# Optimization experiments

Hardware: AMD Instinct MI355X
Metric: run time of the kernel (lower is better)

The kernel has to match this reference:

```python
import jax, jax.numpy as jnp
import numpy as np

B = 4096
FEAT = 512
EMB = 64
HID = 1024
NUM_CLASSES = 64   # == option_num == noise_lib_Y.shape[0]
LIB_X = 256
LIB_Y = 256
OUT_J = 256


def setup_inputs() -> dict:
    key = jax.random.key(0)
    ks = jax.random.split(key, 16)
    s = lambda k, shape, fan: jax.random.normal(k, shape, jnp.float32) / np.sqrt(fan)
    d_in = FEAT + EMB
    return {
        "state": jax.random.normal(ks[0], (B, FEAT), jnp.float32),
        "option": jax.random.randint(ks[1], (B,), 0, NUM_CLASSES, jnp.int64),
        "embed_table": s(ks[2], (NUM_CLASSES, EMB), EMB),
        "Wx1": s(ks[3], (d_in, HID), d_in), "bx1": jnp.zeros((HID,), jnp.float32),
        "Wx2": s(ks[4], (HID, LIB_X), HID), "bx2": jnp.zeros((LIB_X,), jnp.float32),
        "Wy1": s(ks[5], (d_in, HID), d_in), "by1": jnp.zeros((HID,), jnp.float32),
        "Wy2": s(ks[6], (HID, LIB_Y), HID), "by2": jnp.zeros((LIB_Y,), jnp.float32),
        "noise_lib_X": s(ks[7], (LIB_X, OUT_J), LIB_X),
        "noise_lib_Y": s(ks[8], (NUM_CLASSES, LIB_Y, OUT_J), LIB_Y),
    }


def _mlp(x, W1, b1, W2, b2):
    # MLP_RELU, layer_num=2: Linear -> ReLU -> Linear
    h = jax.nn.relu(x @ W1 + b1)
    return h @ W2 + b2


def reference(state, option, embed_table, Wx1, bx1, Wx2, bx2,
              Wy1, by1, Wy2, by2, noise_lib_X, noise_lib_Y):
    option_embed = embed_table[option]                      # [B, EMB]
    all_state = jnp.concatenate([state, option_embed], axis=-1)
    cls_X = _mlp(all_state, Wx1, bx1, Wx2, bx2)             # [B, LIB_X]
    cls_Y = _mlp(all_state, Wy1, by1, Wy2, by2)             # [B, LIB_Y]
    # Original: einsum('bi,mij->bmj') then mask with one_hot(option).
    # Mathematically identical gather-then-matmul (honors the routing sparsity):
    noise_Y_sel = noise_lib_Y[option]                       # [B, LIB_Y, OUT_J]
    generate_noise_Y = jnp.einsum('bi,bij->bj', cls_Y, noise_Y_sel)
    generate_noise_X = cls_X @ noise_lib_X                  # [B, OUT_J]
    return (generate_noise_X, generate_noise_Y)
```

## Files before the change

### kernel.cpp

```cpp
#include <hip/hip_runtime.h>

typedef unsigned short u16;
typedef unsigned int u32;

using f32x4  = __attribute__((ext_vector_type(4))) float;
using bf16x8 = __attribute__((ext_vector_type(8))) __bf16;

#define DEV __device__ __forceinline__

DEV u16 f2bf(float f) {
  union { float f; u32 u; } x; x.f = f;
  return (u16)((x.u + 0x7fffu + ((x.u >> 16) & 1u)) >> 16);
}
DEV float bf2f(u16 h) {
  union { u32 u; float f; } x; x.u = ((u32)h) << 16;
  return x.f;
}

DEV void async_cp16(const u16* g, u16* l) {
  __builtin_amdgcn_global_load_lds((const __attribute__((address_space(1))) void*)g,
                                   (__attribute__((address_space(3))) void*)l,
                                   16, 0, 0);
}

static constexpr int BATCH = 4096;
static constexpr int FEAT  = 512;
static constexpr int EMB   = 64;
static constexpr int HID   = 1024;
static constexpr int NC    = 64;
static constexpr int DIN   = 576;
static constexpr int LIB   = 256;

DEV void detect_lite(const u32* __restrict__ sraw, const u32* __restrict__ oraw,
                     int* isf32, int* ostr) {
  __shared__ int cib, conz;
  const int t = threadIdx.x;
  if (t == 0) { cib = 0; conz = 0; }
  u32 w = sraw[t];
  u32 e = (w >> 7) & 0xFFu;
  unsigned long long m1 = __ballot(e >= 100 && e <= 142);
  unsigned long long m2 = __ballot((t & 1) && oraw[t] != 0);
  __syncthreads();
  if ((t & 63) == 0) {
    atomicAdd(&cib, __popcll(m1));
    atomicAdd(&conz, __popcll(m2));
  }
  __syncthreads();
  *isf32 = (cib < 128) ? 1 : 0;
  *ostr  = (conz == 0) ? 2 : 1;
}

DEV void do_transpose64(const void* __restrict__ in, size_t in_off,
                        u16* __restrict__ out, int R, int C,
                        int by, int bx, int isf32) {
  __shared__ u16 tile[64 * 72];
  const int t = threadIdx.x;
  {
    const int r = t >> 2, c0 = (t & 3) * 16;
    size_t off = in_off + (size_t)(by * 64 + r) * C + (bx * 64 + c0);
    u16 v[16];
    if (isf32) {
      const float4* s = (const float4*)((const float*)in + off);
      float4 a0 = s[0], a1 = s[1], a2 = s[2], a3 = s[3];
      v[0] = f2bf(a0.x); v[1] = f2bf(a0.y); v[2]  = f2bf(a0.z); v[3]  = f2bf(a0.w);
      v[4] = f2bf(a1.x); v[5] = f2bf(a1.y); v[6]  = f2bf(a1.z); v[7]  = f2bf(a1.w);
      v[8] = f2bf(a2.x); v[9] = f2bf(a2.y); v[10] = f2bf(a2.z); v[11] = f2bf(a2.w);
      v[12] = f2bf(a3.x); v[13] = f2bf(a3.y); v[14] = f2bf(a3.z); v[15] = f2bf(a3.w);
    } else {
      const uint4* s = (const uint4*)((const u16*)in + off);
      *(uint4*)&v[0] = s[0];
      *(uint4*)&v[8] = s[1];
    }
    *(uint4*)&tile[r * 72 + c0]     = *(uint4*)&v[0];
    *(uint4*)&tile[r * 72 + c0 + 8] = *(uint4*)&v[8];
  }
  __syncthreads();
  {
    const int c = t & 63, rs = (t >> 6) * 16;
    u16 w[16];
#pragma unroll
    for (int i = 0; i < 16; ++i) w[i] = tile[(rs + i) * 72 + c];
    size_t oo = (size_t)(bx * 64 + c) * R + (by * 64 + rs);
    *(uint4*)&out[oo]     = *(uint4*)&w[0];
    *(uint4*)&out[oo + 8] = *(uint4*)&w[8];
  }
}

struct PrepArgs {
  const void *state, *emb, *Wx1, *Wy1, *Wx2, *Wy2, *nX, *nY;
  const int* opt;
  u16 *all_state, *WT1x, *WT1y, *WT2x, *WT2y, *XT, *YT;
  int *idxs, *offs, *flags;
};
static constexpr int PB_CONCAT = BATCH * 36 / 256;
static constexpr int PB_WT1 = (DIN / 64) * (HID / 64);
static constexpr int PB_WT2 = (HID / 64) * (LIB / 64);
static constexpr int PB_XT  = (LIB / 64) * (LIB / 64);
static constexpr int PB_YT  = PB_XT * NC;
static constexpr int PREP_BLOCKS = 1 + PB_CONCAT + 2 * PB_WT1 + 2 * PB_WT2
                                 + PB_XT + PB_YT;

__global__ __launch_bounds__(256) void prep_k(PrepArgs a) {
  int isf32, os;
  detect_lite((const u32*)a.state, (const u32*)a.opt, &isf32, &os);
  int bid = blockIdx.x;
  if (bid == 0) {
    __shared__ int cnt[NC], cur[NC], offl[NC + 1];
    const int t = threadIdx.x;
    if (t < NC) cnt[t] = 0;
    __syncthreads();
    for (int b = t; b < BATCH; b += 256) atomicAdd(&cnt[a.opt[(size_t)b * os]], 1);
    __syncthreads();
    if (t == 0) {
      int s = 0;
      for (int m = 0; m < NC; ++m) { offl[m] = s; s += cnt[m]; }
      offl[NC] = s;
    }
    __syncthreads();
    if (t < NC) cur[t] = offl[t];
    if (t <= NC) a.offs[t] = offl[t];
    __syncthreads();
    for (int b = t; b < BATCH; b += 256) {
      int p = atomicAdd(&cur[a.opt[(size_t)b * os]], 1);
      a.idxs[p] = b;
    }
    if (t == 0) { a.flags[0] = isf32; a.flags[1] = os; }
    return;
  }
  bid -= 1;
  if (bid < PB_CONCAT) {
    int t = bid * 256 + threadIdx.x;
    int b = t / 36, ch = t % 36;
    const void* base;
    size_t srcoff;
    if (ch < 32) { base = a.state; srcoff = (size_t)b * FEAT + ch * 16; }
    else {
      base = a.emb;
      srcoff = (size_t)a.opt[(size_t)b * os] * EMB + (ch - 32) * 16;
    }
    u16 o[16];
    if (isf32) {
      const float4* s = (const float4*)((const float*)base + srcoff);
      float4 a0 = s[0], a1 = s[1], a2 = s[2], a3 = s[3];
      o[0] = f2bf(a0.x); o[1] = f2bf(a0.y); o[2]  = f2bf(a0.z); o[3]  = f2bf(a0.w);
      o[4] = f2bf(a1.x); o[5] = f2bf(a1.y); o[6]  = f2bf(a1.z); o[7]  = f2bf(a1.w);
      o[8] = f2bf(a2.x); o[9] = f2bf(a2.y); o[10] = f2bf(a2.z); o[11] = f2bf(a2.w);
      o[12] = f2bf(a3.x); o[13] = f2bf(a3.y); o[14] = f2bf(a3.z); o[15] = f2bf(a3.w);
    } else {
      const uint4* s = (const uint4*)((const u16*)base + srcoff);
      *(uint4*)&o[0] = s[0];
      *(uint4*)&o[8] = s[1];
    }
    u16* dst = a.all_state + (size_t)b * DIN + ch * 16;
    *(uint4*)dst       = *(const uint4*)&o[0];
    *(uint4*)(dst + 8) = *(const uint4*)&o[8];
    return;
  }
  bid -= PB_CONCAT;
  if (bid < PB_WT1) { do_transpose64(a.Wx1, 0, a.WT1x, DIN, HID, bid >> 4, bid & 15, isf32); return; }
  bid -= PB_WT1;
  if (bid < PB_WT1) { do_transpose64(a.Wy1, 0, a.WT1y, DIN, HID, bid >> 4, bid & 15, isf32); return; }
  bid -= PB_WT1;
  if (bid < PB_WT2) { do_transpose64(a.Wx2, 0, a.WT2x, HID, LIB, bid >> 2, bid & 3, isf32); return; }
  bid -= PB_WT2;
  if (bid < PB_WT2) { do_transpose64(a.Wy2, 0, a.WT2y, HID, LIB, bid >> 2, bid & 3, isf32); return; }
  bid -= PB_WT2;
  if (bid < PB_XT) { do_transpose64(a.nX, 0, a.XT, LIB, LIB, bid >> 2, bid & 3, isf32); return; }
  bid -= PB_XT;
  {
    int z = bid >> 4, tt = bid & 15;
    do_transpose64(a.nY, (size_t)z * LIB * LIB, a.YT + (size_t)z * LIB * LIB,
                   LIB, LIB, tt >> 2, tt & 3, isf32);
  }
}

struct GArg { const u16* A; const u16* Bt; const void* bias; void* C; int cflag; };

template <int BM, int BN, bool RELU>
__global__ __launch_bounds__(256) void gemm_bt(GArg g0, GArg g1, int M, int N, int K,
                                               const int* __restrict__ flags) {
  constexpr int WM = BM / 2, WN = BN / 2, TM = WM / 16, TN = WN / 16;
  constexpr int AISS = (BM * 32) / 2048, BISS = (BN * 32) / 2048;
  __shared__ __align__(16) u16 As[BM * 32];
  __shared__ __align__(16) u16 Bs[BN * 32];
  const GArg g = blockIdx.z ? g1 : g0;
  const int isf32 = flags[0];
  const bool cf32 = g.cflag && isf32;
  const int t = threadIdx.x;
  const int m0 = blockIdx.y * BM, n0 = blockIdx.x * BN;
  const int lane = t & 63, wid = t >> 6;
  const int wm = wid >> 1, wn = wid & 1;
  const int lr = lane & 15, lq = lane >> 4;
  const int srow = t >> 2, scol = (t & 3) * 8;
  f32x4 acc[TM][TN] = {};
  for (int k0 = 0; k0 < K; k0 += 32) {
    __syncthreads();
#pragma unroll
    for (int s = 0; s < AISS; ++s)
      async_cp16(g.A + (size_t)(m0 + s * 64 + srow) * K + (k0 + scol),
                 &As[s * 2048 + t * 8]);
#pragma unroll
    for (int s = 0; s < BISS; ++s)
      async_cp16(g.Bt + (size_t)(n0 + s * 64 + srow) * K + (k0 + scol),
                 &Bs[s * 2048 + t * 8]);
    __syncthreads();
    bf16x8 av[TM], bv[TN];
#pragma unroll
    for (int i = 0; i < TM; ++i)
      av[i] = *(const bf16x8*)&As[(wm * WM + i * 16 + lr) * 32 + lq * 8];
#pragma unroll
    for (int j = 0; j < TN; ++j)
      bv[j] = *(const bf16x8*)&Bs[(wn * WN + j * 16 + lr) * 32 + lq * 8];
#pragma unroll
    for (int i = 0; i < TM; ++i)
#pragma unroll
      for (int j = 0; j < TN; ++j)
        acc[i][j] = __builtin_amdgcn_mfma_f32_16x16x32_bf16(av[i], bv[j], acc[i][j], 0, 0, 0);
  }
#pragma unroll
  for (int j = 0; j < TN; ++j) {
    const int gc = n0 + wn * WN + j * 16 + lr;
    const float bval = g.bias
        ? (isf32 ? ((const float*)g.bias)[gc] : bf2f(((const u16*)g.bias)[gc]))
        : 0.f;
#pragma unroll
    for (int i = 0; i < TM; ++i) {
      const int gr = m0 + wm * WM + i * 16 + lq * 4;
#pragma unroll
      for (int r = 0; r < 4; ++r) {
        float v = acc[i][j][r] + bval;
        if (RELU) v = fmaxf(v, 0.f);
        const size_t idx = (size_t)(gr + r) * N + gc;
        if (cf32) ((float*)g.C)[idx] = v;
        else      ((u16*)g.C)[idx] = f2bf(v);
      }
    }
  }
}

struct TailArgs {
  const u16 *cls_x, *XT, *cls_y, *YT;
  const int *idxs, *offs, *flags;
  void* out;
};

__global__ __launch_bounds__(256) void tail_k(TailArgs a) {
  __shared__ __align__(16) u16 Bts[64 * 264];
  __shared__ __align__(16) u16 Asm[16 * 264];
  const bool of32 = a.flags[0];
  const int t = threadIdx.x;
  const int lane = t & 63, w = t >> 6, lr = lane & 15, lq = lane >> 4;

  if (blockIdx.x < 256) {
    u16* As = Bts;
    u16* Bs = Bts + 2048;
    const int m0 = (blockIdx.x >> 2) * 64, n0 = (blockIdx.x & 3) * 64;
    const int wm = w >> 1, wn = w & 1;
    const int srow = t >> 2, scol = (t & 3) * 8;
    f32x4 acc[2][2] = {};
    for (int k0 = 0; k0 < LIB; k0 += 32) {
      __syncthreads();
      async_cp16(a.cls_x + (size_t)(m0 + srow) * LIB + (k0 + scol), &As[t * 8]);
      async_cp16(a.XT    + (size_t)(n0 + srow) * LIB + (k0 + scol), &Bs[t * 8]);
      __syncthreads();
      bf16x8 av[2], bv[2];
#pragma unroll
      for (int i = 0; i < 2; ++i)
        av[i] = *(const bf16x8*)&As[(wm * 32 + i * 16 + lr) * 32 + lq * 8];
#pragma unroll
      for (int j = 0; j < 2; ++j)
        bv[j] = *(const bf16x8*)&Bs[(wn * 32 + j * 16 + lr) * 32 + lq * 8];
#pragma unroll
      for (int i = 0; i < 2; ++i)
#pragma unroll
        for (int j = 0; j < 2; ++j)
          acc[i][j] = __builtin_amdgcn_mfma_f32_16x16x32_bf16(av[i], bv[j], acc[i][j], 0, 0, 0);
    }
#pragma unroll
    for (int j = 0; j < 2; ++j) {
      const int gc = n0 + (w & 1) * 32 + j * 16 + lr;
#pragma unroll
      for (int i = 0; i < 2; ++i) {
        const int gr = m0 + (w >> 1) * 32 + i * 16 + lq * 4;
#pragma unroll
        for (int r = 0; r < 4; ++r) {
          const size_t idx = (size_t)(gr + r) * LIB + gc;
          if (of32) ((float*)a.out)[idx] = acc[i][j][r];
          else      ((u16*)a.out)[idx] = f2bf(acc[i][j][r]);
        }
      }
    }
    return;
  }

  const int bid = blockIdx.x - 256;
  const int m = bid >> 2, n0 = (bid & 3) * 64;
  {
    const int r = t >> 2, cb = (t & 3) * 64;
    const u16* src = a.YT + (size_t)m * LIB * LIB + (size_t)(n0 + r) * LIB + cb;
    u16* dst = &Bts[r * 264 + cb];
#pragma unroll
    for (int v = 0; v < 8; ++v)
      *(uint4*)(dst + v * 8) = *(const uint4*)(src + v * 8);
  }
  const int start = a.offs[m], cnt = a.offs[m + 1] - start;
  const size_t out_off = (size_t)BATCH * LIB;
  for (int ch = 0; ch < cnt; ch += 16) {
    __syncthreads();
    {
      const int r = t >> 4, cb = (t & 15) * 16;
      if (ch + r < cnt) {
        const u16* src = a.cls_y + (size_t)a.idxs[start + ch + r] * LIB + cb;
        *(uint4*)&Asm[r * 264 + cb]     = *(const uint4*)src;
        *(uint4*)&Asm[r * 264 + cb + 8] = *(const uint4*)(src + 8);
      } else {
        uint4 z{0, 0, 0, 0};
        *(uint4*)&Asm[r * 264 + cb]     = z;
        *(uint4*)&Asm[r * 264 + cb + 8] = z;
      }
    }
    __syncthreads();
    f32x4 acc = {};
#pragma unroll
    for (int kk = 0; kk < LIB; kk += 32) {
      bf16x8 av = *(const bf16x8*)&Asm[lr * 264 + kk + lq * 8];
      bf16x8 bv = *(const bf16x8*)&Bts[(w * 16 + lr) * 264 + kk + lq * 8];
      acc = __builtin_amdgcn_mfma_f32_16x16x32_bf16(av, bv, acc, 0, 0, 0);
    }
#pragma unroll
    for (int r = 0; r < 4; ++r) {
      const int rowc = lq * 4 + r;
      if (ch + rowc < cnt) {
        const size_t oi = out_off + (size_t)a.idxs[start + ch + rowc] * LIB
                        + (n0 + w * 16 + lr);
        if (of32) ((float*)a.out)[oi] = acc[r];
        else      ((u16*)a.out)[oi] = f2bf(acc[r]);
      }
    }
  }
}

extern "C" void kernel_launch(void* const* d_in, const int* in_sizes, int n_in,
                              void* d_out, int out_size, void* d_ws, size_t ws_size,
                              hipStream_t stream) {
  char* p = (char*)d_ws;
  auto alloc = [&](size_t bytes) { char* r = p; p += (bytes + 255) & ~(size_t)255; return r; };
  int* flags = (int*)alloc(256);
  u16* all_state = (u16*)alloc((size_t)BATCH * DIN * 2);
  u16* h_x   = (u16*)alloc((size_t)BATCH * HID * 2);
  u16* h_y   = (u16*)alloc((size_t)BATCH * HID * 2);
  u16* cls_x = (u16*)alloc((size_t)BATCH * LIB * 2);
  u16* cls_y = (u16*)alloc((size_t)BATCH * LIB * 2);
  u16* WT1x  = (u16*)alloc((size_t)HID * DIN * 2);
  u16* WT1y  = (u16*)alloc((size_t)HID * DIN * 2);
  u16* WT2x  = (u16*)alloc((size_t)LIB * HID * 2);
  u16* WT2y  = (u16*)alloc((size_t)LIB * HID * 2);
  u16* XT    = (u16*)alloc((size_t)LIB * LIB * 2);
  u16* YT    = (u16*)alloc((size_t)NC * LIB * LIB * 2);
  int* idxs  = (int*)alloc((size_t)BATCH * 4);
  int* offs  = (int*)alloc((size_t)(NC + 1) * 4);

  PrepArgs pa;
  pa.state = d_in[0]; pa.opt = (const int*)d_in[1]; pa.emb = d_in[2];
  pa.Wx1 = d_in[3]; pa.Wx2 = d_in[5]; pa.Wy1 = d_in[7]; pa.Wy2 = d_in[9];
  pa.nX = d_in[11]; pa.nY = d_in[12];
  pa.all_state = all_state; pa.WT1x = WT1x; pa.WT1y = WT1y;
  pa.WT2x = WT2x; pa.WT2y = WT2y; pa.XT = XT; pa.YT = YT;
  pa.idxs = idxs; pa.offs = offs; pa.flags = flags;

  prep_k<<<PREP_BLOCKS, 256, 0, stream>>>(pa);

  GArg g1x{all_state, WT1x, d_in[4], h_x, 0}, g1y{all_state, WT1y, d_in[8], h_y, 0};
  gemm_bt<128, 128, true><<<dim3(HID / 128, BATCH / 128, 2), 256, 0, stream>>>(
      g1x, g1y, BATCH, HID, DIN, flags);

  GArg g2x{h_x, WT2x, d_in[6], cls_x, 0}, g2y{h_y, WT2y, d_in[10], cls_y, 0};
  gemm_bt<64, 64, false><<<dim3(LIB / 64, BATCH / 64, 2), 256, 0, stream>>>(
      g2x, g2y, BATCH, LIB, HID, flags);

  TailArgs ta{cls_x, XT, cls_y, YT, idxs, offs, flags, d_out};
  tail_k<<<512, 256, 0, stream>>>(ta);
}
```

Measured before the change: 157.9 us.

## Fuse prep, MLP GEMMs and tail into one persistent kernel with grid barriers

```diff
diff --git a/kernel.cpp b/kernel.cpp
--- a/kernel.cpp
+++ b/kernel.cpp
@@ -30,6 +30,7 @@
 static constexpr int NC    = 64;
 static constexpr int DIN   = 576;
 static constexpr int LIB   = 256;
+static constexpr int NBLK  = 512;
 
 DEV void detect_lite(const u32* __restrict__ sraw, const u32* __restrict__ oraw,
                      int* isf32, int* ostr) {
@@ -50,11 +51,31 @@
   *ostr  = (conz == 0) ? 2 : 1;
 }
 
-DEV void do_transpose64(const void* __restrict__ in, size_t in_off,
+DEV void grid_sync(int* sync, int phase) {
+  __syncthreads();
+  if (threadIdx.x == 0) {
+    __threadfence();
+    int v = __hip_atomic_fetch_add(&sync[phase - 1], 1,
+                                   __ATOMIC_ACQ_REL, __HIP_MEMORY_SCOPE_AGENT);
+    if (v == NBLK - 1) {
+      __hip_atomic_store(&sync[3], phase, __ATOMIC_RELEASE,
+                         __HIP_MEMORY_SCOPE_AGENT);
+    } else {
+      while (__hip_atomic_load(&sync[3], __ATOMIC_ACQUIRE,
+                               __HIP_MEMORY_SCOPE_AGENT) < phase)
+        __builtin_amdgcn_s_sleep(2);
+    }
+    __threadfence();
+  }
+  __syncthreads();
+}
+
+DEV void do_transpose64(u16* lds, const void* __restrict__ in, size_t in_off,
                         u16* __restrict__ out, int R, int C,
                         int by, int bx, int isf32) {
-  __shared__ u16 tile[64 * 72];
+  u16* tile = lds;
   const int t = threadIdx.x;
+  __syncthreads();
   {
     const int r = t >> 2, c0 = (t & 3) * 16;
     size_t off = in_off + (size_t)(by * 64 + r) * C + (bx * 64 + c0);
@@ -86,142 +107,59 @@
   }
 }
 
-struct PrepArgs {
-  const void *state, *emb, *Wx1, *Wy1, *Wx2, *Wy2, *nX, *nY;
-  const int* opt;
-  u16 *all_state, *WT1x, *WT1y, *WT2x, *WT2y, *XT, *YT;
-  int *idxs, *offs, *flags;
-};
-static constexpr int PB_CONCAT = BATCH * 36 / 256;
-static constexpr int PB_WT1 = (DIN / 64) * (HID / 64);
-static constexpr int PB_WT2 = (HID / 64) * (LIB / 64);
-static constexpr int PB_XT  = (LIB / 64) * (LIB / 64);
-static constexpr int PB_YT  = PB_XT * NC;
-static constexpr int PREP_BLOCKS = 1 + PB_CONCAT + 2 * PB_WT1 + 2 * PB_WT2
-                                 + PB_XT + PB_YT;
-
-__global__ __launch_bounds__(256) void prep_k(PrepArgs a) {
-  int isf32, os;
-  detect_lite((const u32*)a.state, (const u32*)a.opt, &isf32, &os);
-  int bid = blockIdx.x;
-  if (bid == 0) {
-    __shared__ int cnt[NC], cur[NC], offl[NC + 1];
-    const int t = threadIdx.x;
-    if (t < NC) cnt[t] = 0;
-    __syncthreads();
-    for (int b = t; b < BATCH; b += 256) atomicAdd(&cnt[a.opt[(size_t)b * os]], 1);
-    __syncthreads();
-    if (t == 0) {
-      int s = 0;
-      for (int m = 0; m < NC; ++m) { offl[m] = s; s += cnt[m]; }
-      offl[NC] = s;
-    }
-    __syncthreads();
-    if (t < NC) cur[t] = offl[t];
-    if (t <= NC) a.offs[t] = offl[t];
-    __syncthreads();
-    for (int b = t; b < BATCH; b += 256) {
-      int p = atomicAdd(&cur[a.opt[(size_t)b * os]], 1);
-      a.idxs[p] = b;
-    }
-    if (t == 0) { a.flags[0] = isf32; a.flags[1] = os; }
-    return;
-  }
-  bid -= 1;
-  if (bid < PB_CONCAT) {
-    int t = bid * 256 + threadIdx.x;
-    int b = t / 36, ch = t % 36;
-    const void* base;
-    size_t srcoff;
-    if (ch < 32) { base = a.state; srcoff = (size_t)b * FEAT + ch * 16; }
-    else {
-      base = a.emb;
-      srcoff = (size_t)a.opt[(size_t)b * os] * EMB + (ch - 32) * 16;
-    }
-    u16 o[16];
-    if (isf32) {
-      const float4* s = (const float4*)((const float*)base + srcoff);
-      float4 a0 = s[0], a1 = s[1], a2 = s[2], a3 = s[3];
-      o[0] = f2bf(a0.x); o[1] = f2bf(a0.y); o[2]  = f2bf(a0.z); o[3]  = f2bf(a0.w);
-      o[4] = f2bf(a1.x); o[5] = f2bf(a1.y); o[6]  = f2bf(a1.z); o[7]  = f2bf(a1.w);
-      o[8] = f2bf(a2.x); o[9] = f2bf(a2.y); o[10] = f2bf(a2.z); o[11] = f2bf(a2.w);
-      o[12] = f2bf(a3.x); o[13] = f2bf(a3.y); o[14] = f2bf(a3.z); o[15] = f2bf(a3.w);
-    } else {
-      const uint4* s = (const uint4*)((const u16*)base + srcoff);
-      *(uint4*)&o[0] = s[0];
-      *(uint4*)&o[8] = s[1];
-    }
-    u16* dst = a.all_state + (size_t)b * DIN + ch * 16;
-    *(uint4*)dst       = *(const uint4*)&o[0];
-    *(uint4*)(dst + 8) = *(const uint4*)&o[8];
-    return;
-  }
-  bid -= PB_CONCAT;
-  if (bid < PB_WT1) { do_transpose64(a.Wx1, 0, a.WT1x, DIN, HID, bid >> 4, bid & 15, isf32); return; }
-  bid -= PB_WT1;
-  if (bid < PB_WT1) { do_transpose64(a.Wy1, 0, a.WT1y, DIN, HID, bid >> 4, bid & 15, isf32); return; }
-  bid -= PB_WT1;
-  if (bid < PB_WT2) { do_transpose64(a.Wx2, 0, a.WT2x, HID, LIB, bid >> 2, bid & 3, isf32); return; }
-  bid -= PB_WT2;
-  if (bid < PB_WT2) { do_transpose64(a.Wy2, 0, a.WT2y, HID, LIB, bid >> 2, bid & 3, isf32); return; }
-  bid -= PB_WT2;
-  if (bid < PB_XT) { do_transpose64(a.nX, 0, a.XT, LIB, LIB, bid >> 2, bid & 3, isf32); return; }
-  bid -= PB_XT;
-  {
-    int z = bid >> 4, tt = bid & 15;
-    do_transpose64(a.nY, (size_t)z * LIB * LIB, a.YT + (size_t)z * LIB * LIB,
-                   LIB, LIB, tt >> 2, tt & 3, isf32);
-  }
-}
-
-struct GArg { const u16* A; const u16* Bt; const void* bias; void* C; int cflag; };
-
 template <int BM, int BN, bool RELU>
-__global__ __launch_bounds__(256) void gemm_bt(GArg g0, GArg g1, int M, int N, int K,
-                                               const int* __restrict__ flags) {
+DEV void gemm_tile(u16* lds, const u16* __restrict__ A, const u16* __restrict__ Bt,
+                   const void* bias, void* C, int N, int K, int m0, int n0,
+                   int isf32, bool cf32) {
   constexpr int WM = BM / 2, WN = BN / 2, TM = WM / 16, TN = WN / 16;
-  constexpr int AISS = (BM * 32) / 2048, BISS = (BN * 32) / 2048;
-  __shared__ __align__(16) u16 As[BM * 32];
-  __shared__ __align__(16) u16 Bs[BN * 32];
-  const GArg g = blockIdx.z ? g1 : g0;
-  const int isf32 = flags[0];
-  const bool cf32 = g.cflag && isf32;
+  u16* As = lds;
+  u16* Bs = lds + BM * 64;
   const int t = threadIdx.x;
-  const int m0 = blockIdx.y * BM, n0 = blockIdx.x * BN;
   const int lane = t & 63, wid = t >> 6;
   const int wm = wid >> 1, wn = wid & 1;
   const int lr = lane & 15, lq = lane >> 4;
-  const int srow = t >> 2, scol = (t & 3) * 8;
   f32x4 acc[TM][TN] = {};
-  for (int k0 = 0; k0 < K; k0 += 32) {
+  for (int k0 = 0; k0 < K; k0 += 64) {
     __syncthreads();
 #pragma unroll
-    for (int s = 0; s < AISS; ++s)
-      async_cp16(g.A + (size_t)(m0 + s * 64 + srow) * K + (k0 + scol),
-                 &As[s * 2048 + t * 8]);
-#pragma unroll
-    for (int s = 0; s < BISS; ++s)
-      async_cp16(g.Bt + (size_t)(n0 + s * 64 + srow) * K + (k0 + scol),
-                 &Bs[s * 2048 + t * 8]);
+    for (int sl = 0; sl < 2; ++sl) {
+#pragma unroll
+      for (int u = 0; u < BM / 64; ++u) {
+        int unit = u * 256 + t;
+        int r = unit >> 2, c8 = (unit & 3) * 8;
+        async_cp16(A + (size_t)(m0 + r) * K + (k0 + sl * 32 + c8),
+                   &As[(sl * BM + r) * 32 + c8]);
+      }
+#pragma unroll
+      for (int u = 0; u < BN / 64; ++u) {
+        int unit = u * 256 + t;
+        int r = unit >> 2, c8 = (unit & 3) * 8;
+        async_cp16(Bt + (size_t)(n0 + r) * K + (k0 + sl * 32 + c8),
+                   &Bs[(sl * BN + r) * 32 + c8]);
+      }
+    }
     __syncthreads();
-    bf16x8 av[TM], bv[TN];
-#pragma unroll
-    for (int i = 0; i < TM; ++i)
-      av[i] = *(const bf16x8*)&As[(wm * WM + i * 16 + lr) * 32 + lq * 8];
-#pragma unroll
-    for (int j = 0; j < TN; ++j)
-      bv[j] = *(const bf16x8*)&Bs[(wn * WN + j * 16 + lr) * 32 + lq * 8];
-#pragma unroll
-    for (int i = 0; i < TM; ++i)
+#pragma unroll
+    for (int sl = 0; sl < 2; ++sl) {
+      bf16x8 av[TM], bv[TN];
+#pragma unroll
+      for (int i = 0; i < TM; ++i)
+        av[i] = *(const bf16x8*)&As[(sl * BM + wm * WM + i * 16 + lr) * 32 + lq * 8];
 #pragma unroll
       for (int j = 0; j < TN; ++j)
-        acc[i][j] = __builtin_amdgcn_mfma_f32_16x16x32_bf16(av[i], bv[j], acc[i][j], 0, 0, 0);
+        bv[j] = *(const bf16x8*)&Bs[(sl * BN + wn * WN + j * 16 + lr) * 32 + lq * 8];
+#pragma unroll
+      for (int i = 0; i < TM; ++i)
+#pragma unroll
+        for (int j = 0; j < TN; ++j)
+          acc[i][j] = __builtin_amdgcn_mfma_f32_16x16x32_bf16(av[i], bv[j], acc[i][j], 0, 0, 0);
+    }
   }
 #pragma unroll
   for (int j = 0; j < TN; ++j) {
     const int gc = n0 + wn * WN + j * 16 + lr;
-    const float bval = g.bias
-        ? (isf32 ? ((const float*)g.bias)[gc] : bf2f(((const u16*)g.bias)[gc]))
+    const float bval = bias
+        ? (isf32 ? ((const float*)bias)[gc] : bf2f(((const u16*)bias)[gc]))
         : 0.f;
 #pragma unroll
     for (int i = 0; i < TM; ++i) {
@@ -231,110 +169,162 @@
         float v = acc[i][j][r] + bval;
         if (RELU) v = fmaxf(v, 0.f);
         const size_t idx = (size_t)(gr + r) * N + gc;
-        if (cf32) ((float*)g.C)[idx] = v;
-        else      ((u16*)g.C)[idx] = f2bf(v);
-      }
-    }
-  }
-}
-
-struct TailArgs {
-  const u16 *cls_x, *XT, *cls_y, *YT;
-  const int *idxs, *offs, *flags;
+        if (cf32) ((float*)C)[idx] = v;
+        else      ((u16*)C)[idx] = f2bf(v);
+      }
+    }
+  }
+}
+
+struct Args {
+  const void *state, *emb, *Wx1, *bx1, *Wx2, *bx2, *Wy1, *by1, *Wy2, *by2, *nX, *nY;
+  const int* opt;
+  u16 *all_state, *h_x, *h_y, *cls_x, *cls_y, *WT1x, *WT1y, *WT2x, *WT2y, *XT, *YT;
   void* out;
+  int* sync;
 };
 
-__global__ __launch_bounds__(256) void tail_k(TailArgs a) {
-  __shared__ __align__(16) u16 Bts[64 * 264];
-  __shared__ __align__(16) u16 Asm[16 * 264];
-  const bool of32 = a.flags[0];
-  const int t = threadIdx.x;
-  const int lane = t & 63, w = t >> 6, lr = lane & 15, lq = lane >> 4;
-
-  if (blockIdx.x < 256) {
-    u16* As = Bts;
-    u16* Bs = Bts + 2048;
-    const int m0 = (blockIdx.x >> 2) * 64, n0 = (blockIdx.x & 3) * 64;
-    const int wm = w >> 1, wn = w & 1;
-    const int srow = t >> 2, scol = (t & 3) * 8;
-    f32x4 acc[2][2] = {};
-    for (int k0 = 0; k0 < LIB; k0 += 32) {
+static constexpr int PT_CONCAT = 576;
+static constexpr int PT_WT1 = 144, PT_WT2 = 64, PT_XT = 16, PT_YT = 1024;
+static constexpr int PT_TOTAL = PT_CONCAT + 2 * PT_WT1 + 2 * PT_WT2
+                              + PT_XT + PT_YT;
+
+__global__ __launch_bounds__(256, 2) void fused_k(Args a) {
+  __shared__ __align__(16) u16 lds[25600];
+  const int t = threadIdx.x, bid = blockIdx.x;
+  int isf32, os;
+  detect_lite((const u32*)a.state, (const u32*)a.opt, &isf32, &os);
+
+  for (int task = bid; task < PT_TOTAL; task += NBLK) {
+    int id = task;
+    if (id < PT_CONCAT) {
+      int idx = id * 256 + t;
+      int b = idx / 36, ch = idx % 36;
+      const void* base;
+      size_t srcoff;
+      if (ch < 32) { base = a.state; srcoff = (size_t)b * FEAT + ch * 16; }
+      else {
+        base = a.emb;
+        srcoff = (size_t)a.opt[(size_t)b * os] * EMB + (ch - 32) * 16;
+      }
+      u16 o[16];
+      if (isf32) {
+        const float4* s = (const float4*)((const float*)base + srcoff);
+        float4 a0 = s[0], a1 = s[1], a2 = s[2], a3 = s[3];
+        o[0] = f2bf(a0.x); o[1] = f2bf(a0.y); o[2]  = f2bf(a0.z); o[3]  = f2bf(a0.w);
+        o[4] = f2bf(a1.x); o[5] = f2bf(a1.y); o[6]  = f2bf(a1.z); o[7]  = f2bf(a1.w);
+        o[8] = f2bf(a2.x); o[9] = f2bf(a2.y); o[10] = f2bf(a2.z); o[11] = f2bf(a2.w);
+        o[12] = f2bf(a3.x); o[13] = f2bf(a3.y); o[14] = f2bf(a3.z); o[15] = f2bf(a3.w);
+      } else {
+        const uint4* s = (const uint4*)((const u16*)base + srcoff);
+        *(uint4*)&o[0] = s[0];
+        *(uint4*)&o[8] = s[1];
+      }
+      u16* dst = a.all_state + (size_t)b * DIN + ch * 16;
+      *(uint4*)dst       = *(const uint4*)&o[0];
+      *(uint4*)(dst + 8) = *(const uint4*)&o[8];
+      continue;
+    }
+    id -= PT_CONCAT;
+    if (id < PT_WT1) { do_transpose64(lds, a.Wx1, 0, a.WT1x, DIN, HID, id >> 4, id & 15, isf32); continue; }
+    id -= PT_WT1;
+    if (id < PT_WT1) { do_transpose64(lds, a.Wy1, 0, a.WT1y, DIN, HID, id >> 4, id & 15, isf32); continue; }
+    id -= PT_WT1;
+    if (id < PT_WT2) { do_transpose64(lds, a.Wx2, 0, a.WT2x, HID, LIB, id >> 2, id & 3, isf32); continue; }
+    id -= PT_WT2;
+    if (id < PT_WT2) { do_transpose64(lds, a.Wy2, 0, a.WT2y, HID, LIB, id >> 2, id & 3, isf32); continue; }
+    id -= PT_WT2;
+    if (id < PT_XT) { do_transpose64(lds, a.nX, 0, a.XT, LIB, LIB, id >> 2, id & 3, isf32); continue; }
+    id -= PT_XT;
+    {
+      int z = id >> 4, sub = id & 15;
+      do_transpose64(lds, a.nY, (size_t)z * LIB * LIB, a.YT + (size_t)z * LIB * LIB,
+                     LIB, LIB, sub >> 2, sub & 3, isf32);
+    }
+  }
+  grid_sync(a.sync, 1);
+
+  {
+    const int head = bid >> 8, r = bid & 255;
+    const int m0 = (r >> 3) * 128, n0 = (r & 7) * 128;
+    gemm_tile<128, 128, true>(lds,
+        a.all_state, head ? a.WT1y : a.WT1x, head ? a.by1 : a.bx1,
+        head ? a.h_y : a.h_x, HID, DIN, m0, n0, isf32, false);
+  }
+  grid_sync(a.sync, 2);
+
+  {
+    const int head = bid >> 8, r = bid & 255;
+    const int m0 = (r >> 2) * 64, n0 = (r & 3) * 64;
+    gemm_tile<64, 64, false>(lds,
+        head ? a.h_y : a.h_x, head ? a.WT2y : a.WT2x, head ? a.by2 : a.bx2,
+        head ? a.cls_y : a.cls_x, LIB, HID, m0, n0, isf32, false);
+  }
+  grid_sync(a.sync, 3);
+
+  const bool of32 = (isf32 != 0);
+  if (bid < 256) {
+    const int m0 = (bid >> 2) * 64, n0 = (bid & 3) * 64;
+    gemm_tile<64, 64, false>(lds, a.cls_x, a.XT, nullptr, a.out,
+                             LIB, LIB, m0, n0, isf32, of32);
+    return;
+  }
+  {
+    u16* Bts = lds;
+    u16* Asm = lds + 16896;
+    u16* list = lds + 21120;
+    __shared__ int lcnt;
+    const int rb = bid - 256;
+    const int m = rb >> 2, n0 = (rb & 3) * 64;
+    const int lane = t & 63, w = t >> 6, lr = lane & 15, lq = lane >> 4;
+    {
+      const int r = t >> 2, cb = (t & 3) * 64;
+      const u16* src = a.YT + (size_t)m * LIB * LIB + (size_t)(n0 + r) * LIB + cb;
+      u16* dst = &Bts[r * 264 + cb];
+#pragma unroll
+      for (int v = 0; v < 8; ++v)
+        *(uint4*)(dst + v * 8) = *(const uint4*)(src + v * 8);
+    }
+    if (t == 0) lcnt = 0;
+    __syncthreads();
+    for (int base = 0; base < BATCH; base += 256) {
+      int e = a.opt[(size_t)(base + t) * os];
+      if (e == m) { int p = atomicAdd(&lcnt, 1); list[p] = (u16)(base + t); }
+    }
+    __syncthreads();
+    const int cnt = lcnt;
+    const size_t out_off = (size_t)BATCH * LIB;
+    for (int ch = 0; ch < cnt; ch += 16) {
       __syncthreads();
-      async_cp16(a.cls_x + (size_t)(m0 + srow) * LIB + (k0 + scol), &As[t * 8]);
-      async_cp16(a.XT    + (size_t)(n0 + srow) * LIB + (k0 + scol), &Bs[t * 8]);
+      {
+        const int r = t >> 4, cb = (t & 15) * 16;
+        if (ch + r < cnt) {
+          const u16* src = a.cls_y + (size_t)list[ch + r] * LIB + cb;
+          *(uint4*)&Asm[r * 264 + cb]     = *(const uint4*)src;
+          *(uint4*)&Asm[r * 264 + cb + 8] = *(const uint4*)(src + 8);
+        } else {
+          uint4 z{0, 0, 0, 0};
+          *(uint4*)&Asm[r * 264 + cb]     = z;
+          *(uint4*)&Asm[r * 264 + cb + 8] = z;
+        }
+      }
       __syncthreads();
-      bf16x8 av[2], bv[2];
-#pragma unroll
-      for (int i = 0; i < 2; ++i)
-        av[i] = *(const bf16x8*)&As[(wm * 32 + i * 16 + lr) * 32 + lq * 8];
-#pragma unroll
-      for (int j = 0; j < 2; ++j)
-        bv[j] = *(const bf16x8*)&Bs[(wn * 32 + j * 16 + lr) * 32 + lq * 8];
-#pragma unroll
-      for (int i = 0; i < 2; ++i)
-#pragma unroll
-        for (int j = 0; j < 2; ++j)
-          acc[i][j] = __builtin_amdgcn_mfma_f32_16x16x32_bf16(av[i], bv[j], acc[i][j], 0, 0, 0);
-    }
-#pragma unroll
-    for (int j = 0; j < 2; ++j) {
-      const int gc = n0 + (w & 1) * 32 + j * 16 + lr;
-#pragma unroll
-      for (int i = 0; i < 2; ++i) {
-        const int gr = m0 + (w >> 1) * 32 + i * 16 + lq * 4;
-#pragma unroll
-        for (int r = 0; r < 4; ++r) {
-          const size_t idx = (size_t)(gr + r) * LIB + gc;
-          if (of32) ((float*)a.out)[idx] = acc[i][j][r];
-          else      ((u16*)a.out)[idx] = f2bf(acc[i][j][r]);
+      f32x4 acc = {};
+#pragma unroll
+      for (int kk = 0; kk < LIB; kk += 32) {
+        bf16x8 av = *(const bf16x8*)&Asm[lr * 264 + kk + lq * 8];
+        bf16x8 bv = *(const bf16x8*)&Bts[(w * 16 + lr) * 264 + kk + lq * 8];
+        acc = __builtin_amdgcn_mfma_f32_16x16x32_bf16(av, bv, acc, 0, 0, 0);
+      }
+#pragma unroll
+      for (int r = 0; r < 4; ++r) {
+        const int rowc = lq * 4 + r;
+        if (ch + rowc < cnt) {
+          const size_t oi = out_off + (size_t)list[ch + rowc] * LIB
+                          + (n0 + w * 16 + lr);
+          if (of32) ((float*)a.out)[oi] = acc[r];
+          else      ((u16*)a.out)[oi] = f2bf(acc[r]);
         }
-      }
-    }
-    return;
-  }
-
-  const int bid = blockIdx.x - 256;
-  const int m = bid >> 2, n0 = (bid & 3) * 64;
-  {
-    const int r = t >> 2, cb = (t & 3) * 64;
-    const u16* src = a.YT + (size_t)m * LIB * LIB + (size_t)(n0 + r) * LIB + cb;
-    u16* dst = &Bts[r * 264 + cb];
-#pragma unroll
-    for (int v = 0; v < 8; ++v)
-      *(uint4*)(dst + v * 8) = *(const uint4*)(src + v * 8);
-  }
-  const int start = a.offs[m], cnt = a.offs[m + 1] - start;
-  const size_t out_off = (size_t)BATCH * LIB;
-  for (int ch = 0; ch < cnt; ch += 16) {
-    __syncthreads();
-    {
-      const int r = t >> 4, cb = (t & 15) * 16;
-      if (ch + r < cnt) {
-        const u16* src = a.cls_y + (size_t)a.idxs[start + ch + r] * LIB + cb;
-        *(uint4*)&Asm[r * 264 + cb]     = *(const uint4*)src;
-        *(uint4*)&Asm[r * 264 + cb + 8] = *(const uint4*)(src + 8);
-      } else {
-        uint4 z{0, 0, 0, 0};
-        *(uint4*)&Asm[r * 264 + cb]     = z;
-        *(uint4*)&Asm[r * 264 + cb + 8] = z;
-      }
-    }
-    __syncthreads();
-    f32x4 acc = {};
-#pragma unroll
-    for (int kk = 0; kk < LIB; kk += 32) {
-      bf16x8 av = *(const bf16x8*)&Asm[lr * 264 + kk + lq * 8];
-      bf16x8 bv = *(const bf16x8*)&Bts[(w * 16 + lr) * 264 + kk + lq * 8];
-      acc = __builtin_amdgcn_mfma_f32_16x16x32_bf16(av, bv, acc, 0, 0, 0);
-    }
-#pragma unroll
-    for (int r = 0; r < 4; ++r) {
-      const int rowc = lq * 4 + r;
-      if (ch + rowc < cnt) {
-        const size_t oi = out_off + (size_t)a.idxs[start + ch + rowc] * LIB
-                        + (n0 + w * 16 + lr);
-        if (of32) ((float*)a.out)[oi] = acc[r];
-        else      ((u16*)a.out)[oi] = f2bf(acc[r]);
       }
     }
   }
@@ -345,7 +335,7 @@
                               hipStream_t stream) {
   char* p = (char*)d_ws;
   auto alloc = [&](size_t bytes) { char* r = p; p += (bytes + 255) & ~(size_t)255; return r; };
-  int* flags = (int*)alloc(256);
+  int* sync  = (int*)alloc(64);
   u16* all_state = (u16*)alloc((size_t)BATCH * DIN * 2);
   u16* h_x   = (u16*)alloc((size_t)BATCH * HID * 2);
   u16* h_y   = (u16*)alloc((size_t)BATCH * HID * 2);
@@ -357,27 +347,18 @@
   u16* WT2y  = (u16*)alloc((size_t)LIB * HID * 2);
   u16* XT    = (u16*)alloc((size_t)LIB * LIB * 2);
   u16* YT    = (u16*)alloc((size_t)NC * LIB * LIB * 2);
-  int* idxs  = (int*)alloc((size_t)BATCH * 4);
-  int* offs  = (int*)alloc((size_t)(NC + 1) * 4);
-
-  PrepArgs pa;
-  pa.state = d_in[0]; pa.opt = (const int*)d_in[1]; pa.emb = d_in[2];
-  pa.Wx1 = d_in[3]; pa.Wx2 = d_in[5]; pa.Wy1 = d_in[7]; pa.Wy2 = d_in[9];
-  pa.nX = d_in[11]; pa.nY = d_in[12];
-  pa.all_state = all_state; pa.WT1x = WT1x; pa.WT1y = WT1y;
-  pa.WT2x = WT2x; pa.WT2y = WT2y; pa.XT = XT; pa.YT = YT;
-  pa.idxs = idxs; pa.offs = offs; pa.flags = flags;
-
-  prep_k<<<PREP_BLOCKS, 256, 0, stream>>>(pa);
-
-  GArg g1x{all_state, WT1x, d_in[4], h_x, 0}, g1y{all_state, WT1y, d_in[8], h_y, 0};
-  gemm_bt<128, 128, true><<<dim3(HID / 128, BATCH / 128, 2), 256, 0, stream>>>(
-      g1x, g1y, BATCH, HID, DIN, flags);
-
-  GArg g2x{h_x, WT2x, d_in[6], cls_x, 0}, g2y{h_y, WT2y, d_in[10], cls_y, 0};
-  gemm_bt<64, 64, false><<<dim3(LIB / 64, BATCH / 64, 2), 256, 0, stream>>>(
-      g2x, g2y, BATCH, LIB, HID, flags);
-
-  TailArgs ta{cls_x, XT, cls_y, YT, idxs, offs, flags, d_out};
-  tail_k<<<512, 256, 0, stream>>>(ta);
-}
+
+  Args a;
+  a.state = d_in[0]; a.opt = (const int*)d_in[1]; a.emb = d_in[2];
+  a.Wx1 = d_in[3]; a.bx1 = d_in[4]; a.Wx2 = d_in[5]; a.bx2 = d_in[6];
+  a.Wy1 = d_in[7]; a.by1 = d_in[8]; a.Wy2 = d_in[9]; a.by2 = d_in[10];
+  a.nX = d_in[11]; a.nY = d_in[12];
+  a.all_state = all_state; a.h_x = h_x; a.h_y = h_y;
+  a.cls_x = cls_x; a.cls_y = cls_y;
+  a.WT1x = WT1x; a.WT1y = WT1y; a.WT2x = WT2x; a.WT2y = WT2y;
+  a.XT = XT; a.YT = YT;
+  a.out = d_out; a.sync = sync;
+
+  hipMemsetAsync(sync, 0, 64, stream);
+  fused_k<<<NBLK, 256, 0, stream>>>(a);
+}
```

Result: slower. 392.7 us (+148.7%).
